# Kernel optimization log

Measured on AMD Instinct MI355X. Metric: run time of the kernel, lower is better.

Reference implementation:

```python
import jax, jax.numpy as jnp
import numpy as np

H = 64          # nheads
NH = 8          # lru_dim // nheads (per-head state dim, must be even)
LRU_DIM = 512
HIDDEN = 512
BATCH = 8
T = 4096
MAX_PHASE = 6.28
R_MIN, R_MAX = 0.9, 0.999


def setup_inputs() -> dict:
    key = jax.random.key(0)
    ks = jax.random.split(key, 8)
    input_sequence = jax.random.normal(ks[0], (BATCH, 1, HIDDEN, 1, T), dtype=jnp.float32)
    # theta_init: log(uniform(0, max_phase)), shape (lru_dim//2, 1)
    theta_log = jnp.log(jax.random.uniform(ks[1], (LRU_DIM // 2, 1), maxval=MAX_PHASE))
    # ortho_mat_init(lru_dim, N)
    P = jax.random.normal(ks[2], (LRU_DIM, NH)) / jnp.sqrt(NH + LRU_DIM)
    # mat_init(lru_dim, hidden_dim)
    B = jax.random.normal(ks[3], (LRU_DIM, HIDDEN)) / jnp.sqrt(HIDDEN + LRU_DIM)
    # mat_init(hidden_dim, lru_dim)
    C = jax.random.normal(ks[4], (HIDDEN, LRU_DIM)) / jnp.sqrt(HIDDEN + LRU_DIM)
    D = jax.random.normal(ks[5], (HIDDEN,))
    # nu_log_init: log(-log r) interpolated by uniform
    u1 = jax.random.uniform(ks[6], (H,))
    gamma_log = jnp.log(-jnp.log(R_MAX)) + u1 * (jnp.log(-jnp.log(R_MIN)) - jnp.log(-jnp.log(R_MAX)))
    return dict(input_sequence=input_sequence, theta_log=theta_log, P=P, B=B, C=C, D=D,
                gamma_log=gamma_log)


def _mix_sequence(gamma, thetas, Us):
    """Single head. gamma: scalar, thetas: (N/2,), Us: (T, B, N) -> (T, B, N)."""
    def binf(a, b):
        g_i, th_i, acc_i = a
        g_j, th_j, acc_j = b
        # rotate-half (RoPE-style) of accumulated state
        rot = jnp.stack([-acc_i[..., 1::2], acc_i[..., 0::2]], axis=-1).reshape(acc_i.shape)
        theta = jnp.repeat(th_j[..., None], 2, axis=-1).reshape(th_j.shape[:-1] + (th_j.shape[-1] * 2,))
        sin = jnp.sin(theta)[..., None, :]  # (..., 1, N)
        cos = jnp.cos(theta)[..., None, :]
        acc = g_j[..., None, None] * (cos * acc_i + sin * rot)
        return (g_i * g_j, th_i + th_j, acc + acc_j)

    Tlen = Us.shape[0]
    gammas = jnp.repeat(gamma[None], Tlen, axis=0)          # (T,)
    Rs = jnp.repeat(thetas[None, :], Tlen, axis=0)          # (T, N/2)
    _, _, res = jax.lax.associative_scan(binf, (gammas, Rs, Us))
    return res


def reference(input_sequence, theta_log, P, B, C, D, gamma_log):
    x = input_sequence[:, 0, :, 0].transpose(0, 2, 1)       # (B, T, hidden)
    bsz, Tlen, _ = x.shape
    thetas = jnp.exp(theta_log.reshape(H, NH // 2))          # (H, N/2)
    Pm = P.reshape(H, NH, NH)
    Bm = B.reshape(H, NH, HIDDEN)
    gamma = jnp.exp(-jnp.exp(gamma_log))                     # (H,)
    # trace(B B^T) per head == sum of squares
    trace_per_head = jnp.sum(Bm * Bm, axis=(1, 2))
    norm = jnp.sqrt((1.0 - gamma ** 2) / trace_per_head)
    B_norm = norm[:, None, None] * Bm                        # (H, N, hidden)
    # orthogonalize P via matrix exponential of skew-symmetric part
    Pm = jax.vmap(jax.scipy.linalg.expm)(Pm - Pm.transpose(0, 2, 1))  # (H, N, N)
    Us = jnp.einsum('HnD,BTD->HTBn', B_norm, x)              # project inputs per head
    Us = jnp.einsum('HnN,HTBn->HTBN', Pm.transpose(0, 2, 1), Us)
    y = jax.vmap(_mix_sequence)(gamma, thetas, Us)           # (H, T, B, N)
    y = jnp.einsum('HNn,HTBN->HTBn', Pm, y)
    y = y.transpose(2, 1, 0, 3).reshape(bsz, Tlen, -1)       # (B, T, lru_dim)
    y = jnp.einsum('Dn,BTn->BTD', C, y) + D * x
    return y[0]                                              # (T, hidden)
```

## Files before the change

### kernel.cpp

```cpp
#include <hip/hip_runtime.h>
#include <math.h>

#define NHEADS   64
#define TLEN     4096
#define CHUNK    16
#define NCHUNK   256

typedef unsigned short u16;
typedef unsigned int   u32;
typedef __attribute__((ext_vector_type(8))) short bf16x8;
typedef __attribute__((ext_vector_type(4))) float f32x4;

__device__ __forceinline__ u16 f2bf(float x) {
    u32 u = __float_as_uint(x);
    u32 r = (u + 0x7FFFu + ((u >> 16) & 1u)) >> 16;
    return (u16)r;
}
__device__ __forceinline__ float bf2f(u16 h) { return __uint_as_float(((u32)h) << 16); }


__global__ void k_pre(const float* __restrict__ X, u16* __restrict__ XT,
                      const float* __restrict__ P,
                      const float* __restrict__ Bmat,
                      const float* __restrict__ theta_log,
                      const float* __restrict__ gamma_log,
                      float* __restrict__ ws) {
    const int tid = threadIdx.x;
    if (blockIdx.x < 512) {
        __shared__ float Xs[64][65];
        const int t0 = (blockIdx.x & 63) * 64, d0 = (blockIdx.x >> 6) * 64;
        {
            const int dr = tid >> 4, tc = (tid & 15) * 4;
            #pragma unroll
            for (int it = 0; it < 4; ++it) {
                const int dd = it*16 + dr;
                float4 v = *reinterpret_cast<const float4*>(X + (size_t)(d0 + dd)*4096 + t0 + tc);
                Xs[dd][tc] = v.x; Xs[dd][tc+1] = v.y; Xs[dd][tc+2] = v.z; Xs[dd][tc+3] = v.w;
            }
        }
        __syncthreads();
        const int tr = tid >> 2, ds = (tid & 3) * 16;
        u32 hb[8], lb[8];
        #pragma unroll
        for (int j = 0; j < 16; j += 2) {
            float a = Xs[ds + j][tr], b = Xs[ds + j + 1][tr];
            u16 ha = f2bf(a), la = f2bf(a - bf2f(ha));
            u16 hbb = f2bf(b), lbb = f2bf(b - bf2f(hbb));
            hb[j >> 1] = (u32)ha | ((u32)hbb << 16);
            lb[j >> 1] = (u32)la | ((u32)lbb << 16);
        }
        u16* orow = XT + (size_t)(t0 + tr)*1024 + d0 + ds;
        uint4 h0; h0.x = hb[0]; h0.y = hb[1]; h0.z = hb[2]; h0.w = hb[3];
        uint4 h1; h1.x = hb[4]; h1.y = hb[5]; h1.z = hb[6]; h1.w = hb[7];
        uint4 l0; l0.x = lb[0]; l0.y = lb[1]; l0.z = lb[2]; l0.w = lb[3];
        uint4 l1; l1.x = lb[4]; l1.y = lb[5]; l1.z = lb[6]; l1.w = lb[7];
        *reinterpret_cast<uint4*>(orow)       = h0;
        *reinterpret_cast<uint4*>(orow + 8)   = h1;
        *reinterpret_cast<uint4*>(orow + 512) = l0;
        *reinterpret_cast<uint4*>(orow + 520) = l1;
        return;
    }
    __shared__ double As[8][8];
    __shared__ double Rs[8][8];
    __shared__ double red[256];
    __shared__ int sh_s;
    const int h = blockIdx.x - 512;
    const int i = (tid & 63) >> 3, j = tid & 7;
    const bool act = tid < 64;

    if (act)
        As[i][j] = (double)P[(h*8 + i)*8 + j] - (double)P[(h*8 + j)*8 + i];

    const float* Bh = Bmat + h*8*512;
    double ss = 0.0;
    #pragma unroll
    for (int q = 0; q < 16; ++q) { float v = Bh[q*256 + tid]; ss += (double)v * (double)v; }
    red[tid] = ss;
    __syncthreads();

    if (tid == 0) {
        double nrm = 0.0;
        for (int r = 0; r < 8; ++r) {
            double rs = 0.0;
            for (int c = 0; c < 8; ++c) rs += fabs(As[r][c]);
            nrm = fmax(nrm, rs);
        }
        int s = 0;
        while (nrm > 0.25 && s < 40) { nrm *= 0.5; ++s; }
        sh_s = s;
        double tr = 0.0;
        for (int q = 0; q < 256; ++q) tr += red[q];
        double ed = exp((double)gamma_log[h]);
        double g  = exp(-ed);
        ws[4096 + h] = (float)g;
        ws[4416 + h] = (float)sqrt((1.0 - g*g) / tr);
    }
    if (tid < 4) ws[4160 + h*4 + tid] = expf(theta_log[h*4 + tid]);
    __syncthreads();

    const int NT = 13;
    if (act) {
        const double sc = ldexp(1.0, -sh_s);
        As[i][j] *= sc;
        Rs[i][j] = (i == j ? 1.0 : 0.0) + As[i][j] / (double)NT;
    }
    __syncthreads();
    for (int k = NT - 1; k >= 1; --k) {
        double t = 0.0;
        if (act) {
            #pragma unroll
            for (int m = 0; m < 8; ++m) t += As[i][m] * Rs[m][j];
        }
        __syncthreads();
        if (act) Rs[i][j] = (i == j ? 1.0 : 0.0) + t / (double)k;
        __syncthreads();
    }
    const int nsq = sh_s;
    for (int q = 0; q < nsq; ++q) {
        double t = 0.0;
        if (act) {
            #pragma unroll
            for (int m = 0; m < 8; ++m) t += Rs[i][m] * Rs[m][j];
        }
        __syncthreads();
        if (act) Rs[i][j] = t;
        __syncthreads();
    }
    if (act) ws[h*64 + i*8 + j] = (float)Rs[i][j];
}

__global__ void k_proj(const float* __restrict__ Bmat,
                       const float* __restrict__ C,
                       const float* __restrict__ ws_ro,
                       u16* __restrict__ W1pk,
                       u16* __restrict__ CEpk) {
    const int gid = blockIdx.x * 256 + threadIdx.x;
    if (gid < 512*512) {
        const int k = gid >> 9, d = gid & 511;
        const int h = k >> 3, N = k & 7;
        const float* Pm = ws_ro + h*64 + N*8;
        const float nrm = ws_ro[4416 + h];
        float acc = 0.f;
        #pragma unroll
        for (int n = 0; n < 8; ++n) acc += Pm[n] * Bmat[(h*8 + n)*512 + d];
        acc *= nrm;
        u16 hi = f2bf(acc), lo = f2bf(acc - bf2f(hi));
        W1pk[k*1024 + d] = hi;
        W1pk[k*1024 + 512 + d] = lo;
    } else {
        const int g2 = gid - 512*512;
        const int e = g2 >> 9, k = g2 & 511;
        const int h = k >> 3, N = k & 7;
        const float* Pm = ws_ro + h*64 + N*8;
        float acc = 0.f;
        #pragma unroll
        for (int n = 0; n < 8; ++n) acc += Pm[n] * C[e*512 + h*8 + n];
        u16 hi = f2bf(acc), lo = f2bf(acc - bf2f(hi));
        CEpk[e*1024 + k] = hi;
        CEpk[e*1024 + 512 + k] = lo;
    }
}

#define MFMA_BF16(A_, B_, C_) __builtin_amdgcn_mfma_f32_16x16x32_bf16(A_, B_, C_, 0, 0, 0)
template<int MODE>
__global__ __launch_bounds__(256) void k_gemm(const u16* __restrict__ Apk,
                                              const float* __restrict__ Af,
                                              const u16* __restrict__ Bpk,
                                              float* __restrict__ Cout,
                                              const u16* __restrict__ XT,
                                              const float* __restrict__ Dvec,
                                              const float* __restrict__ wsro,
                                              float* __restrict__ E,
                                              const float* __restrict__ S,
                                              const float* __restrict__ TAB) {
    __shared__ char smem[36864];
    u16* Ah = (u16*)smem;
    u16* Al = Ah + 4608;
    u16* Bh = Al + 4608;
    u16* Bl = Bh + 4608;
    float* Ut = (float*)smem;

    const int tid = threadIdx.x;
    const int bid = blockIdx.x;
    const int tile = (bid & 7) * 64 + (bid >> 3);
    const int mt = tile >> 3, nt = tile & 7;
    const int m0 = mt * 64, n0 = nt * 64;
    const int lane = tid & 63, wid = tid >> 6;
    const int wm = wid >> 1, wn = wid & 1;
    const int lr = lane & 15, lc = lane >> 4;
    const int sr = tid >> 2, ss = (tid & 3) * 16;

    f32x4 acc00 = {0.f,0.f,0.f,0.f}, acc01 = acc00, acc10 = acc00, acc11 = acc00;

    const int tA = m0 + sr;
    const int cA = tA >> 4, iA = tA & 15;
    const u16* Brow = Bpk + (size_t)(n0 + sr)*1024 + ss;
    const u16* Arow = (MODE == 0) ? (Apk + (size_t)tA*1024 + ss) : (const u16*)0;
    const float* Urow = (MODE == 1) ? (Af + (size_t)tA*512 + ss) : (const float*)0;

    float4 rb0, rb1, rb2, rb3;
    float4 ra0, ra1, ra2, ra3;
    float4 ru[4], rtb[4], rsv[4];

    {
        const int k0 = 0;
        rb0 = *reinterpret_cast<const float4*>(Brow + k0);
        rb1 = *reinterpret_cast<const float4*>(Brow + k0 + 8);
        rb2 = *reinterpret_cast<const float4*>(Brow + 512 + k0);
        rb3 = *reinterpret_cast<const float4*>(Brow + 512 + k0 + 8);
        if constexpr (MODE == 0) {
            ra0 = *reinterpret_cast<const float4*>(Arow + k0);
            ra1 = *reinterpret_cast<const float4*>(Arow + k0 + 8);
            ra2 = *reinterpret_cast<const float4*>(Arow + 512 + k0);
            ra3 = *reinterpret_cast<const float4*>(Arow + 512 + k0 + 8);
        } else {
            const int p0 = (k0 + ss) >> 1;
            #pragma unroll
            for (int j = 0; j < 4; ++j) {
                ru[j]  = *reinterpret_cast<const float4*>(Urow + k0 + 4*j);
                rtb[j] = *reinterpret_cast<const float4*>(TAB + ((size_t)iA*256 + p0 + 2*j)*2);
                rsv[j] = *reinterpret_cast<const float4*>(S + (size_t)cA*512 + 2*p0 + 4*j);
            }
        }
    }

    for (int s = 0; s < 8; ++s) {
        if constexpr (MODE == 0) {
            *reinterpret_cast<float4*>(&Ah[sr*72 + ss])     = ra0;
            *reinterpret_cast<float4*>(&Ah[sr*72 + ss + 8]) = ra1;
            *reinterpret_cast<float4*>(&Al[sr*72 + ss])     = ra2;
            *reinterpret_cast<float4*>(&Al[sr*72 + ss + 8]) = ra3;
        } else {
            #pragma unroll
            for (int j = 0; j < 4; ++j) {
                float4 u = ru[j], tb = rtb[j], sv = rsv[j];
                u.x += tb.x*sv.x - tb.y*sv.y;
                u.y += tb.y*sv.x + tb.x*sv.y;
                u.z += tb.z*sv.z - tb.w*sv.w;
                u.w += tb.w*sv.z + tb.z*sv.w;
                u16 hx = f2bf(u.x), hy = f2bf(u.y), hz = f2bf(u.z), hw = f2bf(u.w);
                u16 lx = f2bf(u.x - bf2f(hx)), ly = f2bf(u.y - bf2f(hy));
                u16 lz = f2bf(u.z - bf2f(hz)), lw = f2bf(u.w - bf2f(hw));
                uint2 wh; wh.x = (u32)hx | ((u32)hy << 16); wh.y = (u32)hz | ((u32)hw << 16);
                uint2 wl; wl.x = (u32)lx | ((u32)ly << 16); wl.y = (u32)lz | ((u32)lw << 16);
                *reinterpret_cast<uint2*>(&Ah[sr*72 + ss + 4*j]) = wh;
                *reinterpret_cast<uint2*>(&Al[sr*72 + ss + 4*j]) = wl;
            }
        }
        *reinterpret_cast<float4*>(&Bh[sr*72 + ss])     = rb0;
        *reinterpret_cast<float4*>(&Bh[sr*72 + ss + 8]) = rb1;
        *reinterpret_cast<float4*>(&Bl[sr*72 + ss])     = rb2;
        *reinterpret_cast<float4*>(&Bl[sr*72 + ss + 8]) = rb3;
        __syncthreads();

        if (s < 7) {
            const int k0 = (s + 1) * 64;
            rb0 = *reinterpret_cast<const float4*>(Brow + k0);
            rb1 = *reinterpret_cast<const float4*>(Brow + k0 + 8);
            rb2 = *reinterpret_cast<const float4*>(Brow + 512 + k0);
            rb3 = *reinterpret_cast<const float4*>(Brow + 512 + k0 + 8);
            if constexpr (MODE == 0) {
                ra0 = *reinterpret_cast<const float4*>(Arow + k0);
                ra1 = *reinterpret_cast<const float4*>(Arow + k0 + 8);
                ra2 = *reinterpret_cast<const float4*>(Arow + 512 + k0);
                ra3 = *reinterpret_cast<const float4*>(Arow + 512 + k0 + 8);
            } else {
                const int p0 = (k0 + ss) >> 1;
                #pragma unroll
                for (int j = 0; j < 4; ++j) {
                    ru[j]  = *reinterpret_cast<const float4*>(Urow + k0 + 4*j);
                    rtb[j] = *reinterpret_cast<const float4*>(TAB + ((size_t)iA*256 + p0 + 2*j)*2);
                    rsv[j] = *reinterpret_cast<const float4*>(S + (size_t)cA*512 + 2*p0 + 4*j);
                }
            }
        }

        #pragma unroll
        for (int kk = 0; kk < 2; ++kk) {
            const int ko = kk*32 + lc*8;
            const int ra0i = (wm*32 + lr)*72 + ko,  ra1i = ra0i + 16*72;
            const int rb0i = (wn*32 + lr)*72 + ko,  rb1i = rb0i + 16*72;
            bf16x8 fah0 = *reinterpret_cast<const bf16x8*>(&Ah[ra0i]);
            bf16x8 fah1 = *reinterpret_cast<const bf16x8*>(&Ah[ra1i]);
            bf16x8 fal0 = *reinterpret_cast<const bf16x8*>(&Al[ra0i]);
            bf16x8 fal1 = *reinterpret_cast<const bf16x8*>(&Al[ra1i]);
            bf16x8 fbh0 = *reinterpret_cast<const bf16x8*>(&Bh[rb0i]);
            bf16x8 fbh1 = *reinterpret_cast<const bf16x8*>(&Bh[rb1i]);
            bf16x8 fbl0 = *reinterpret_cast<const bf16x8*>(&Bl[rb0i]);
            bf16x8 fbl1 = *reinterpret_cast<const bf16x8*>(&Bl[rb1i]);
            acc00 = MFMA_BF16(fah0, fbl0, acc00);
            acc00 = MFMA_BF16(fal0, fbh0, acc00);
            acc00 = MFMA_BF16(fah0, fbh0, acc00);
            acc01 = MFMA_BF16(fah0, fbl1, acc01);
            acc01 = MFMA_BF16(fal0, fbh1, acc01);
            acc01 = MFMA_BF16(fah0, fbh1, acc01);
            acc10 = MFMA_BF16(fah1, fbl0, acc10);
            acc10 = MFMA_BF16(fal1, fbh0, acc10);
            acc10 = MFMA_BF16(fah1, fbh0, acc10);
            acc11 = MFMA_BF16(fah1, fbl1, acc11);
            acc11 = MFMA_BF16(fal1, fbh1, acc11);
            acc11 = MFMA_BF16(fah1, fbh1, acc11);
        }
        __syncthreads();
    }

    if constexpr (MODE == 0) {
        #pragma unroll
        for (int im = 0; im < 2; ++im) {
            #pragma unroll
            for (int in = 0; in < 2; ++in) {
                f32x4 v = (im == 0) ? (in == 0 ? acc00 : acc01)
                                    : (in == 0 ? acc10 : acc11);
                const int row0 = wm*32 + im*16 + lc*4;
                const int col  = wn*32 + in*16 + lr;
                #pragma unroll
                for (int rg = 0; rg < 4; ++rg)
                    Ut[(row0 + rg)*72 + col] = v[rg];
            }
        }
        __syncthreads();
        if (tid < 128) {
            const int cc = tid >> 5, pp = tid & 31;
            const int pg = nt*32 + pp;
            const float th = wsro[4160 + pg];
            const float g  = wsro[4096 + (pg >> 2)];
            const float cs = cosf(th), sn = sinf(th);
            float h0 = 0.f, h1 = 0.f;
            float* col = Ut + (cc*16)*72 + 2*pp;
            #pragma unroll
            for (int i = 0; i < CHUNK; ++i) {
                float a = col[i*72], b = col[i*72 + 1];
                float n0v = g*(cs*h0 - sn*h1) + a;
                float n1v = g*(sn*h0 + cs*h1) + b;
                col[i*72] = n0v; col[i*72 + 1] = n1v;
                h0 = n0v; h1 = n1v;
            }
            E[(size_t)(mt*4 + cc)*512 + 2*pg]     = h0;
            E[(size_t)(mt*4 + cc)*512 + 2*pg + 1] = h1;
        }
        __syncthreads();
        const int row = tid >> 2, cseg = (tid & 3) * 16;
        #pragma unroll
        for (int j = 0; j < 4; ++j) {
            float4 v = *reinterpret_cast<const float4*>(&Ut[row*72 + cseg + 4*j]);
            *reinterpret_cast<float4*>(Cout + (size_t)(m0 + row)*512 + n0 + cseg + 4*j) = v;
        }
    } else {
        #pragma unroll
        for (int im = 0; im < 2; ++im) {
            #pragma unroll
            for (int in = 0; in < 2; ++in) {
                f32x4 v = (im == 0) ? (in == 0 ? acc00 : acc01)
                                    : (in == 0 ? acc10 : acc11);
                const int row0 = m0 + wm*32 + im*16 + lc*4;
                const int col  = n0 + wn*32 + in*16 + lr;
                const float dv = Dvec[col];
                #pragma unroll
                for (int rg = 0; rg < 4; ++rg) {
                    const int t = row0 + rg;
                    float xv = bf2f(XT[(size_t)t*1024 + col]) + bf2f(XT[(size_t)t*1024 + 512 + col]);
                    Cout[(size_t)t*512 + col] = v[rg] + dv*xv;
                }
            }
        }
    }
}

__global__ void k_carry(const float* __restrict__ E, float* __restrict__ S,
                        float* __restrict__ TAB,
                        const float* __restrict__ theta_log,
                        const float* __restrict__ gamma_log) {
    const int w = threadIdx.x >> 6, l = threadIdx.x & 63;
    const int p = blockIdx.x*4 + w;
    const double th = exp((double)theta_log[p]);
    const double ed = exp((double)gamma_log[p >> 2]);

    if (l < CHUNK) {
        double a = (double)(l + 1) * th;
        double g = exp(-(double)(l + 1) * ed);
        TAB[((size_t)l*256 + p)*2 + 0] = (float)(g * cos(a));
        TAB[((size_t)l*256 + p)*2 + 1] = (float)(g * sin(a));
    }

    const double a16 = 16.0*th, g16 = exp(-16.0*ed);
    const float Lc = (float)(g16*cos(a16)), Ls = (float)(g16*sin(a16));

    const float* Ep = E + 2*p;
    float2 e0 = *reinterpret_cast<const float2*>(Ep + (size_t)(4*l + 0)*512);
    float2 e1 = *reinterpret_cast<const float2*>(Ep + (size_t)(4*l + 1)*512);
    float2 e2 = *reinterpret_cast<const float2*>(Ep + (size_t)(4*l + 2)*512);
    float2 e3 = *reinterpret_cast<const float2*>(Ep + (size_t)(4*l + 3)*512);

    float2 v = e0;
    v = make_float2(Lc*v.x - Ls*v.y + e1.x, Ls*v.x + Lc*v.y + e1.y);
    v = make_float2(Lc*v.x - Ls*v.y + e2.x, Ls*v.x + Lc*v.y + e2.y);
    v = make_float2(Lc*v.x - Ls*v.y + e3.x, Ls*v.x + Lc*v.y + e3.y);

    #pragma unroll
    for (int d = 0; d < 6; ++d) {
        const int sh = 1 << d;
        const double aa = 64.0 * (double)sh * th;
        const double gg = exp(-64.0 * (double)sh * ed);
        const float Mc = (float)(gg*cos(aa)), Ms = (float)(gg*sin(aa));
        float px = __shfl_up(v.x, sh, 64);
        float py = __shfl_up(v.y, sh, 64);
        if (l >= sh) {
            v.x += Mc*px - Ms*py;
            v.y += Ms*px + Mc*py;
        }
    }

    float sx = __shfl_up(v.x, 1, 64), sy = __shfl_up(v.y, 1, 64);
    float2 s = (l == 0) ? make_float2(0.f, 0.f) : make_float2(sx, sy);
    float* Sp = S + 2*p;
    *reinterpret_cast<float2*>(Sp + (size_t)(4*l + 0)*512) = s;
    s = make_float2(Lc*s.x - Ls*s.y + e0.x, Ls*s.x + Lc*s.y + e0.y);
    *reinterpret_cast<float2*>(Sp + (size_t)(4*l + 1)*512) = s;
    s = make_float2(Lc*s.x - Ls*s.y + e1.x, Ls*s.x + Lc*s.y + e1.y);
    *reinterpret_cast<float2*>(Sp + (size_t)(4*l + 2)*512) = s;
    s = make_float2(Lc*s.x - Ls*s.y + e2.x, Ls*s.x + Lc*s.y + e2.y);
    *reinterpret_cast<float2*>(Sp + (size_t)(4*l + 3)*512) = s;
}

extern "C" void kernel_launch(void* const* d_in, const int* in_sizes, int n_in,
                              void* d_out, int out_size, void* d_ws, size_t ws_size,
                              hipStream_t stream) {
    const float* X  = (const float*)d_in[0];
    const float* th = (const float*)d_in[1];
    const float* P  = (const float*)d_in[2];
    const float* Bm = (const float*)d_in[3];
    const float* C  = (const float*)d_in[4];
    const float* Dv = (const float*)d_in[5];
    const float* gl = (const float*)d_in[6];
    char* wsb = (char*)d_ws;
    float* ws   = (float*)wsb;
    u16*   W1pk = (u16*)(wsb + 32768);
    u16*   CEpk = (u16*)(wsb + 1081344);
    u16*   XTpk = (u16*)(wsb + 2129920);
    float* U    = (float*)(wsb + 10518528);
    float* E    = (float*)(wsb + 18907136);
    float* S    = (float*)(wsb + 19431424);
    float* TAB  = (float*)(wsb + 19955712);
    float* out  = (float*)d_out;

    k_pre<<<576, 256, 0, stream>>>(X, XTpk, P, Bm, th, gl, ws);
    k_proj<<<2048, 256, 0, stream>>>(Bm, C, ws, W1pk, CEpk);
    k_gemm<0><<<512, 256, 0, stream>>>(XTpk, (const float*)0, W1pk, U, XTpk, Dv, ws, E, S, TAB);
    k_carry<<<64, 256, 0, stream>>>(E, S, TAB, th, gl);
    k_gemm<1><<<512, 256, 0, stream>>>((const u16*)0, U, CEpk, out, XTpk, Dv, ws, E, S, TAB);
}
```

Measured before the change: 149.1 us.

## Double-buffer LDS tiles in k_gemm and truncate low bf16 residual

Restructures the GEMM main loop to use two LDS buffers, so the next tile is stored while MFMAs run on the current one. This cuts the barriers per k-step from two to one. It also raises the launch-bounds occupancy hint to 2 and switches the low-part bf16 conversion of the split-precision A operand to plain truncation, which saves ALU work. The costs are double the shared memory (72KB per block), which may limit occupancy, and a slight precision loss in the low residual.

```diff
diff --git a/kernel.cpp b/kernel.cpp
--- a/kernel.cpp
+++ b/kernel.cpp
@@ -17,6 +17,7 @@
     return (u16)r;
 }
 __device__ __forceinline__ float bf2f(u16 h) { return __uint_as_float(((u32)h) << 16); }
+__device__ __forceinline__ u16 f2bf_trunc(float x) { return (u16)(__float_as_uint(x) >> 16); }
 
 
 __global__ void k_pre(const float* __restrict__ X, u16* __restrict__ XT,
@@ -163,21 +164,17 @@
 
 #define MFMA_BF16(A_, B_, C_) __builtin_amdgcn_mfma_f32_16x16x32_bf16(A_, B_, C_, 0, 0, 0)
 template<int MODE>
-__global__ __launch_bounds__(256) void k_gemm(const u16* __restrict__ Apk,
-                                              const float* __restrict__ Af,
-                                              const u16* __restrict__ Bpk,
-                                              float* __restrict__ Cout,
-                                              const u16* __restrict__ XT,
-                                              const float* __restrict__ Dvec,
-                                              const float* __restrict__ wsro,
-                                              float* __restrict__ E,
-                                              const float* __restrict__ S,
-                                              const float* __restrict__ TAB) {
-    __shared__ char smem[36864];
-    u16* Ah = (u16*)smem;
-    u16* Al = Ah + 4608;
-    u16* Bh = Al + 4608;
-    u16* Bl = Bh + 4608;
+__global__ __launch_bounds__(256, 2) void k_gemm(const u16* __restrict__ Apk,
+                                                 const float* __restrict__ Af,
+                                                 const u16* __restrict__ Bpk,
+                                                 float* __restrict__ Cout,
+                                                 const u16* __restrict__ XT,
+                                                 const float* __restrict__ Dvec,
+                                                 const float* __restrict__ wsro,
+                                                 float* __restrict__ E,
+                                                 const float* __restrict__ S,
+                                                 const float* __restrict__ TAB) {
+    __shared__ char smem[73728];
     float* Ut = (float*)smem;
 
     const int tid = threadIdx.x;
@@ -202,8 +199,7 @@
     float4 ra0, ra1, ra2, ra3;
     float4 ru[4], rtb[4], rsv[4];
 
-    {
-        const int k0 = 0;
+    auto LOADREGS = [&](int k0) {
         rb0 = *reinterpret_cast<const float4*>(Brow + k0);
         rb1 = *reinterpret_cast<const float4*>(Brow + k0 + 8);
         rb2 = *reinterpret_cast<const float4*>(Brow + 512 + k0);
@@ -222,9 +218,8 @@
                 rsv[j] = *reinterpret_cast<const float4*>(S + (size_t)cA*512 + 2*p0 + 4*j);
             }
         }
-    }
-
-    for (int s = 0; s < 8; ++s) {
+    };
+    auto STORE = [&](u16* Ah, u16* Al, u16* Bh, u16* Bl) {
         if constexpr (MODE == 0) {
             *reinterpret_cast<float4*>(&Ah[sr*72 + ss])     = ra0;
             *reinterpret_cast<float4*>(&Ah[sr*72 + ss + 8]) = ra1;
@@ -239,8 +234,8 @@
                 u.z += tb.z*sv.z - tb.w*sv.w;
                 u.w += tb.w*sv.z + tb.z*sv.w;
                 u16 hx = f2bf(u.x), hy = f2bf(u.y), hz = f2bf(u.z), hw = f2bf(u.w);
-                u16 lx = f2bf(u.x - bf2f(hx)), ly = f2bf(u.y - bf2f(hy));
-                u16 lz = f2bf(u.z - bf2f(hz)), lw = f2bf(u.w - bf2f(hw));
+                u16 lx = f2bf_trunc(u.x - bf2f(hx)), ly = f2bf_trunc(u.y - bf2f(hy));
+                u16 lz = f2bf_trunc(u.z - bf2f(hz)), lw = f2bf_trunc(u.w - bf2f(hw));
                 uint2 wh; wh.x = (u32)hx | ((u32)hy << 16); wh.y = (u32)hz | ((u32)hw << 16);
                 uint2 wl; wl.x = (u32)lx | ((u32)ly << 16); wl.y = (u32)lz | ((u32)lw << 16);
                 *reinterpret_cast<uint2*>(&Ah[sr*72 + ss + 4*j]) = wh;
@@ -251,30 +246,8 @@
         *reinterpret_cast<float4*>(&Bh[sr*72 + ss + 8]) = rb1;
         *reinterpret_cast<float4*>(&Bl[sr*72 + ss])     = rb2;
         *reinterpret_cast<float4*>(&Bl[sr*72 + ss + 8]) = rb3;
-        __syncthreads();
-
-        if (s < 7) {
-            const int k0 = (s + 1) * 64;
-            rb0 = *reinterpret_cast<const float4*>(Brow + k0);
-            rb1 = *reinterpret_cast<const float4*>(Brow + k0 + 8);
-            rb2 = *reinterpret_cast<const float4*>(Brow + 512 + k0);
-            rb3 = *reinterpret_cast<const float4*>(Brow + 512 + k0 + 8);
-            if constexpr (MODE == 0) {
-                ra0 = *reinterpret_cast<const float4*>(Arow + k0);
-                ra1 = *reinterpret_cast<const float4*>(Arow + k0 + 8);
-                ra2 = *reinterpret_cast<const float4*>(Arow + 512 + k0);
-                ra3 = *reinterpret_cast<const float4*>(Arow + 512 + k0 + 8);
-            } else {
-                const int p0 = (k0 + ss) >> 1;
-                #pragma unroll
-                for (int j = 0; j < 4; ++j) {
-                    ru[j]  = *reinterpret_cast<const float4*>(Urow + k0 + 4*j);
-                    rtb[j] = *reinterpret_cast<const float4*>(TAB + ((size_t)iA*256 + p0 + 2*j)*2);
-                    rsv[j] = *reinterpret_cast<const float4*>(S + (size_t)cA*512 + 2*p0 + 4*j);
-                }
-            }
-        }
-
+    };
+    auto MFMAS = [&](const u16* Ah, const u16* Al, const u16* Bh, const u16* Bl) {
         #pragma unroll
         for (int kk = 0; kk < 2; ++kk) {
             const int ko = kk*32 + lc*8;
@@ -301,6 +274,22 @@
             acc11 = MFMA_BF16(fal1, fbh1, acc11);
             acc11 = MFMA_BF16(fah1, fbh1, acc11);
         }
+    };
+
+    u16* buf0 = (u16*)smem;
+    u16* buf1 = (u16*)(smem + 36864);
+
+    LOADREGS(0);
+    STORE(buf0, buf0 + 4608, buf0 + 9216, buf0 + 13824);
+    __syncthreads();
+
+    #pragma unroll
+    for (int s = 0; s < 8; ++s) {
+        u16* bp = (s & 1) ? buf1 : buf0;
+        u16* bq = (s & 1) ? buf0 : buf1;
+        if (s < 7) LOADREGS((s + 1) * 64);
+        MFMAS(bp, bp + 4608, bp + 9216, bp + 13824);
+        if (s < 7) STORE(bq, bq + 4608, bq + 9216, bq + 13824);
         __syncthreads();
     }
 
```

Result: no change. 148.2 us, median of 2 (-0.6%).
